# Kernel optimization log

Hardware: AMD Instinct MI355X
Metric: run time of the kernel (lower is better)

## Reference

```python
import jax, jax.numpy as jnp
import numpy as np
import math

B, H, N, D = 2, 16, 2048, 128
SM_SCALE = 1.0 / math.sqrt(D)


def setup_inputs() -> dict:
    key = jax.random.key(0)
    kq, kk, kv = jax.random.split(key, 3)
    q = jax.random.normal(kq, (B, H, N, D), dtype=jnp.float32)
    k = jax.random.normal(kk, (B, H, N, D), dtype=jnp.float32)
    v = jax.random.normal(kv, (B, H, N, D), dtype=jnp.float32)
    return {"q": q, "k": k, "v": v}


def reference(q, k, v):
    # RBF-kernel causal attention (non-softmax):
    #   logits_ij = -sm_scale * ||q_i - k_j||^2
    #            = 2*sm_scale*q_i.k_j - sm_scale*||q_i||^2 - sm_scale*||k_j||^2
    #   p = exp(logits) with causal mask (p_ij = 0 for j > i); out = p @ v
    sm_scale = jnp.float32(SM_SCALE)
    q_sq = sm_scale * jnp.sum(q * q, axis=-1)  # [B,H,N]
    k_sq = sm_scale * jnp.sum(k * k, axis=-1)  # [B,H,N]
    qk = jnp.einsum("bhmd,bhnd->bhmn", q, k)
    logits = (2.0 * sm_scale) * qk - q_sq[..., :, None] - k_sq[..., None, :]
    n = q.shape[2]
    causal = jnp.tril(jnp.ones((n, n), dtype=bool))
    logits = jnp.where(causal, logits, -jnp.inf)
    p = jnp.exp(logits)  # NOT normalized (non-softmax attention)
    out = jnp.einsum("bhmn,bhnd->bhmd", p, v)
    return out
```

## Files before the change

### kernel.cpp

```cpp
#include <hip/hip_runtime.h>
#include <math.h>


#define NSEQ 2048
#define DH   128
#define BHC  32
#define SM_SCALE 0.08838834764831845f

typedef __attribute__((ext_vector_type(8))) short    short8;
typedef __attribute__((ext_vector_type(8))) _Float16 half8;
typedef __attribute__((ext_vector_type(4))) short    short4_;
typedef __attribute__((ext_vector_type(4))) float    float4_;
typedef __attribute__((ext_vector_type(4))) unsigned uint4_;
typedef __attribute__((ext_vector_type(2))) unsigned uint2_;

#define KST 136
#define VST 72
#define PST 72

__device__ __forceinline__ short f2bf(float x){
  union{float f; unsigned u;} a; a.f=x;
  unsigned r = a.u + 0x7fffu + ((a.u>>16)&1u);
  return (short)(r>>16);
}
__device__ __forceinline__ float bf2f(short h){
  union{float f; unsigned u;} a; a.u=((unsigned)(unsigned short)h)<<16; return a.f;
}
__device__ __forceinline__ unsigned packbf(float a, float b){
  return (unsigned)(unsigned short)f2bf(a) | ((unsigned)(unsigned short)f2bf(b)<<16);
}

__global__ __launch_bounds__(256)
void prep_kv5(const float* __restrict__ kg, const float* __restrict__ vg,
              _Float16* __restrict__ khg, short* __restrict__ vtg,
              float* __restrict__ ksqg){
  __shared__ unsigned Vls[128*33];
  const int b = blockIdx.x, t = threadIdx.x;
  const int l = t & 63, wv = t >> 6;
  if(b < 1024){
    const int bh = b>>5, jt = b&31;
    const float4_* vb4 = (const float4_*)(vg + ((size_t)bh*NSEQ + (size_t)jt*64)*DH);
    #pragma unroll
    for(int i=0;i<8;++i){
      float4_ own = vb4[i*256 + t];
      float4_ par;
      par.x = __shfl_xor(own.x, 32); par.y = __shfl_xor(own.y, 32);
      par.z = __shfl_xor(own.z, 32); par.w = __shfl_xor(own.w, 32);
      const int hi = (l>>5)&1;
      unsigned w0 = hi ? packbf(par.z, own.z) : packbf(own.x, par.x);
      unsigned w1 = hi ? packbf(par.w, own.w) : packbf(own.y, par.y);
      const int dd = 4*(t&31) + 2*hi;
      const int j2 = 4*i + wv;
      Vls[dd*33 + j2]     = w0;
      Vls[(dd+1)*33 + j2] = w1;
    }
    __syncthreads();
    short* outp = vtg + ((size_t)(bh*32 + jt)*DH)*64;
    #pragma unroll
    for(int it=0; it<4; ++it){
      int idx = t + 256*it;
      int d = idx>>3, slot = idx&7;
      uint4_ o;
      o.x = Vls[d*33 + 4*slot];   o.y = Vls[d*33 + 4*slot+1];
      o.z = Vls[d*33 + 4*slot+2]; o.w = Vls[d*33 + 4*slot+3];
      *(uint4_*)(outp + d*64 + 8*slot) = o;
    }
  } else {
    const int kb = b - 1024;
    const float4_* kb4 = (const float4_*)(kg + (size_t)kb*64*DH);
    #pragma unroll
    for(int i=0;i<8;++i){
      float4_ x = kb4[i*256 + t];
      const int row = 64*kb + 8*i + (t>>5);
      const int d   = 4*(t&31);
      union{ _Float16 h[4]; uint2_ u; } pk;
      pk.h[0]=(_Float16)x.x; pk.h[1]=(_Float16)x.y;
      pk.h[2]=(_Float16)x.z; pk.h[3]=(_Float16)x.w;
      *(uint2_*)(khg + (size_t)row*DH + d) = pk.u;
      float ss = x.x*x.x + x.y*x.y + x.z*x.z + x.w*x.w;
      ss += __shfl_xor(ss,1);  ss += __shfl_xor(ss,2);
      ss += __shfl_xor(ss,4);  ss += __shfl_xor(ss,8);
      ss += __shfl_xor(ss,16);
      if((l&31)==0) ksqg[row] = SM_SCALE*ss;
    }
  }
}

__global__ __launch_bounds__(256,2)
void rbf_attn5(const float* __restrict__ qg,
               const _Float16* __restrict__ khg,
               const short* __restrict__ vtg,
               const float* __restrict__ ksqg,
               float* __restrict__ og){
  __shared__ short Kst[64*KST];
  __shared__ short Vst[128*VST];
  __shared__ short Pls[4*32*PST];
  __shared__ float ksLs[64];

  const int tid=threadIdx.x;
  const int w=tid>>6, l=tid&63;
  const int quad=l>>4, lr=l&15;
  const int bh=blockIdx.x, y=blockIdx.y;
  const int s = (y<8) ? y : 23-y;
  const int m_w   = (w<2) ? s : 31-s;
  const int qbase = 64*m_w + 32*(w&1);
  const int mb = 31-s;

  const float*    Qg = qg   + (size_t)bh*NSEQ*DH;
  const _Float16* Kh = khg  + (size_t)bh*NSEQ*DH;
  const short*    Vt = vtg  + (size_t)bh*32*DH*64;
  const float*    Ks = ksqg + (size_t)bh*NSEQ;
  float*          Og = og   + (size_t)bh*NSEQ*DH;
  short* Pw = Pls + w*32*PST;

  half8 qf[2][4];
  float qsq[2];
  #pragma unroll
  for(int rt=0;rt<2;++rt){
    const int qrow = qbase + 16*rt + lr;
    const float* qp = Qg + (size_t)qrow*DH + 8*quad;
    float ss=0.f;
    #pragma unroll
    for(int ks=0;ks<4;++ks){
      float4_ a = *(const float4_*)(qp + 32*ks);
      float4_ b = *(const float4_*)(qp + 32*ks + 4);
      half8 h;
      #pragma unroll
      for(int j=0;j<4;++j){
        h[j]   = (_Float16)a[j];
        h[j+4] = (_Float16)b[j];
        ss += a[j]*a[j] + b[j]*b[j];
      }
      qf[rt][ks]=h;
    }
    ss += __shfl_xor(ss,16);
    ss += __shfl_xor(ss,32);
    qsq[rt] = SM_SCALE*ss;
  }

  float4_ oacc[2][8];
  #pragma unroll
  for(int a=0;a<2;++a)
    #pragma unroll
    for(int b=0;b<8;++b) oacc[a][b] = (float4_)0.f;

  uint4_ kreg[4], vreg[4];
  float  kqreg = 0.f;
  {
    #pragma unroll
    for(int it=0;it<4;++it){
      int idx = tid + 256*it;
      int row = idx>>4, c = idx&15;
      kreg[it] = *(const uint4_*)(Kh + (size_t)row*DH + 8*c);
      int d = idx>>3, slot = idx&7;
      vreg[it] = *(const uint4_*)(Vt + (size_t)d*64 + 8*slot);
    }
    if(tid<64) kqreg = Ks[tid];
  }

  for(int jt=0; jt<=mb; ++jt){
    #pragma unroll
    for(int it=0;it<4;++it){
      int idx = tid + 256*it;
      int row = idx>>4, c = idx&15;
      *(uint4_*)&Kst[row*KST + 8*c] = kreg[it];
      int d = idx>>3, slot = idx&7;
      *(uint4_*)&Vst[d*VST + 8*slot] = vreg[it];
    }
    if(tid<64) ksLs[tid] = kqreg;
    __syncthreads();

    if(jt < mb){
      const int jc2 = (jt+1)*64;
      #pragma unroll
      for(int it=0;it<4;++it){
        int idx = tid + 256*it;
        int row = idx>>4, c = idx&15;
        kreg[it] = *(const uint4_*)(Kh + (size_t)(jc2+row)*DH + 8*c);
        int d = idx>>3, slot = idx&7;
        vreg[it] = *(const uint4_*)(Vt + ((size_t)(jt+1)*DH + d)*64 + 8*slot);
      }
      if(tid<64) kqreg = Ks[jc2 + tid];
    }

    if(jt <= m_w){
      float4_ sacc[2][4];
      #pragma unroll
      for(int a=0;a<2;++a)
        #pragma unroll
        for(int b=0;b<4;++b) sacc[a][b] = (float4_)0.f;

      #pragma unroll
      for(int ks=0;ks<4;++ks){
        half8 kf[4];
        #pragma unroll
        for(int ct=0;ct<4;++ct)
          kf[ct] = *(const half8*)&Kst[(16*ct+lr)*KST + 32*ks + 8*quad];
        #pragma unroll
        for(int rt=0;rt<2;++rt)
          #pragma unroll
          for(int ct=0;ct<4;++ct)
            sacc[rt][ct]=__builtin_amdgcn_mfma_f32_16x16x32_f16(kf[ct],qf[rt][ks],sacc[rt][ct],0,0,0);
      }

      const int jg0 = 64*jt;
      #pragma unroll
      for(int rt=0;rt<2;++rt){
        const int qrow = qbase + 16*rt + lr;
        const float qs = qsq[rt];
        #pragma unroll
        for(int ct=0;ct<4;++ct){
          float4_ kq = *(const float4_*)&ksLs[16*ct + 4*quad];
          const int j0 = jg0 + 16*ct + 4*quad;
          short4_ pw;
          #pragma unroll
          for(int r=0;r<4;++r){
            float logit = (2.f*SM_SCALE)*sacc[rt][ct][r] - qs - kq[r];
            float p = (j0 + r <= qrow) ? __expf(logit) : 0.f;
            pw[r] = f2bf(p);
          }
          *(short4_*)&Pw[(16*rt+lr)*PST + 16*ct + 4*quad] = pw;
        }
      }

      #pragma unroll
      for(int ks2=0;ks2<2;++ks2){
        short8 pf[2];
        #pragma unroll
        for(int rt=0;rt<2;++rt)
          pf[rt] = *(const short8*)&Pw[(16*rt+lr)*PST + 32*ks2 + 8*quad];
        #pragma unroll
        for(int ctv=0;ctv<8;++ctv){
          const short8 vf = *(const short8*)&Vst[(16*ctv+lr)*VST + 32*ks2 + 8*quad];
          #pragma unroll
          for(int rt=0;rt<2;++rt)
            oacc[rt][ctv]=__builtin_amdgcn_mfma_f32_16x16x32_bf16(pf[rt],vf,oacc[rt][ctv],0,0,0);
        }
      }
    }
    __syncthreads();
  }

  #pragma unroll
  for(int rt=0;rt<2;++rt)
    #pragma unroll
    for(int ctv=0;ctv<8;++ctv)
      #pragma unroll
      for(int r=0;r<4;++r){
        const int qrow = qbase + 16*rt + 4*quad + r;
        Og[(size_t)qrow*DH + 16*ctv + lr] = oacc[rt][ctv][r];
      }
}

#define KSTf 136
#define VSTf 36
#define PSTf 72

__global__ __launch_bounds__(256,2)
void rbf_attn_mfma(const float* __restrict__ qg, const float* __restrict__ kg,
                   const float* __restrict__ vg, float* __restrict__ og){
  __shared__ short    Khi[64*KSTf];
  __shared__ short    Klo[64*KSTf];
  __shared__ unsigned VP [128*VSTf];
  __shared__ short    Pfb[64*PSTf];
  __shared__ float    qsq_s[64];
  __shared__ float    ksq_s[64];

  const int tid=threadIdx.x;
  const int w=tid>>6, l=tid&63;
  const int wr=w>>1, wc=w&1;
  const int quad=l>>4, lr=l&15;
  const int bh=blockIdx.x, yp=blockIdx.y;

  const float* Qg = qg + (size_t)bh*NSEQ*DH;
  const float* Kg = kg + (size_t)bh*NSEQ*DH;
  const float* Vg = vg + (size_t)bh*NSEQ*DH;
  float*       Og = og + (size_t)bh*NSEQ*DH;

  for(int pass=0;pass<2;++pass){
    const int m = pass ? (31-yp) : yp;
    __syncthreads();
    short8 qhf[2][4], qlf[2][4];
    #pragma unroll
    for(int rt=0;rt<2;++rt){
      const int grow = m*64 + 32*wr + 16*rt + lr;
      const float* qp = Qg + (size_t)grow*DH + 8*quad;
      float ss=0.f;
      #pragma unroll
      for(int ks=0;ks<4;++ks){
        float4_ a = *(const float4_*)(qp + 32*ks);
        float4_ b = *(const float4_*)(qp + 32*ks + 4);
        short8 hi, lo;
        #pragma unroll
        for(int j=0;j<4;++j){
          float fa=a[j], fb=b[j];
          short ha=f2bf(fa); hi[j]=ha;   lo[j]=f2bf(fa-bf2f(ha));
          short hb=f2bf(fb); hi[j+4]=hb; lo[j+4]=f2bf(fb-bf2f(hb));
          ss += fa*fa + fb*fb;
        }
        qhf[rt][ks]=hi; qlf[rt][ks]=lo;
      }
      ss += __shfl_xor(ss,16);
      ss += __shfl_xor(ss,32);
      if(wc==0 && quad==0) qsq_s[32*wr+16*rt+lr] = SM_SCALE*ss;
    }
    float4_ oacc[2][4];
    #pragma unroll
    for(int a=0;a<2;++a)
      #pragma unroll
      for(int b=0;b<4;++b) oacc[a][b] = (float4_)0.f;

    const int ntiles = m+1;
    for(int jt=0;jt<ntiles;++jt){
      const int jc = jt*64;
      __syncthreads();
      #pragma unroll
      for(int it=0;it<4;++it){
        const int i = tid + 256*it;
        const int row = i>>4, c0 = 8*(i&15);
        const float* kp = Kg + (size_t)(jc+row)*DH + c0;
        float4_ a = *(const float4_*)kp;
        float4_ b = *(const float4_*)(kp+4);
        short8 hi, lo;
        float ss=0.f;
        #pragma unroll
        for(int j=0;j<4;++j){
          float fa=a[j], fb=b[j];
          short ha=f2bf(fa); hi[j]=ha;   lo[j]=f2bf(fa-bf2f(ha));
          short hb=f2bf(fb); hi[j+4]=hb; lo[j+4]=f2bf(fb-bf2f(hb));
          ss += fa*fa + fb*fb;
        }
        ss += __shfl_xor(ss,1); ss += __shfl_xor(ss,2);
        ss += __shfl_xor(ss,4); ss += __shfl_xor(ss,8);
        if(lr==0) ksq_s[row] = SM_SCALE*ss;
        *(short8*)&Khi[row*KSTf + c0] = hi;
        *(short8*)&Klo[row*KSTf + c0] = lo;
      }
      #pragma unroll
      for(int it=0;it<4;++it){
        const int u = tid + 256*it;
        const int d = u & 127, jg = u >> 7;
        const float* vp = Vg + (size_t)(jc + 8*jg)*DH + d;
        float vv[8];
        #pragma unroll
        for(int jj=0;jj<8;++jj) vv[jj] = vp[(size_t)jj*DH];
        uint4_ pk;
        #pragma unroll
        for(int p2=0;p2<4;++p2)
          pk[p2] = (unsigned)(unsigned short)f2bf(vv[2*p2]) |
                   ((unsigned)(unsigned short)f2bf(vv[2*p2+1])<<16);
        *(uint4_*)&VP[d*VSTf + 4*jg] = pk;
      }
      __syncthreads();
      float4_ sacc[2][2];
      #pragma unroll
      for(int a=0;a<2;++a)
        #pragma unroll
        for(int b=0;b<2;++b) sacc[a][b] = (float4_)0.f;
      #pragma unroll
      for(int ks=0;ks<4;++ks){
        short8 khf[2], klf[2];
        #pragma unroll
        for(int ct=0;ct<2;++ct){
          const int off = (32*wc + 16*ct + lr)*KSTf + 32*ks + 8*quad;
          khf[ct] = *(const short8*)&Khi[off];
          klf[ct] = *(const short8*)&Klo[off];
        }
        #pragma unroll
        for(int rt=0;rt<2;++rt)
          #pragma unroll
          for(int ct=0;ct<2;++ct){
            sacc[rt][ct]=__builtin_amdgcn_mfma_f32_16x16x32_bf16(qhf[rt][ks],khf[ct],sacc[rt][ct],0,0,0);
            sacc[rt][ct]=__builtin_amdgcn_mfma_f32_16x16x32_bf16(qhf[rt][ks],klf[ct],sacc[rt][ct],0,0,0);
            sacc[rt][ct]=__builtin_amdgcn_mfma_f32_16x16x32_bf16(qlf[rt][ks],khf[ct],sacc[rt][ct],0,0,0);
          }
      }
      #pragma unroll
      for(int rt=0;rt<2;++rt){
        float qs[4];
        #pragma unroll
        for(int r=0;r<4;++r) qs[r]=qsq_s[32*wr+16*rt+4*quad+r];
        #pragma unroll
        for(int ct=0;ct<2;++ct){
          const float ksq = ksq_s[32*wc+16*ct+lr];
          const int colg = jc + 32*wc+16*ct+lr;
          #pragma unroll
          for(int r=0;r<4;++r){
            const int rowg = m*64 + 32*wr+16*rt+4*quad+r;
            float logit = (2.f*SM_SCALE)*sacc[rt][ct][r] - qs[r] - ksq;
            float p = (colg<=rowg)? __expf(logit) : 0.f;
            Pfb[(32*wr+16*rt+4*quad+r)*PSTf + 32*wc+16*ct+lr] = f2bf(p);
          }
        }
      }
      __syncthreads();
      #pragma unroll
      for(int ks2=0;ks2<2;++ks2){
        short8 pf[2];
        #pragma unroll
        for(int rt=0;rt<2;++rt)
          pf[rt] = *(const short8*)&Pfb[(32*wr+16*rt+lr)*PSTf + 32*ks2 + 8*quad];
        #pragma unroll
        for(int ctv=0;ctv<4;++ctv){
          const int d = 64*wc + 16*ctv + lr;
          const short8 vfb = *(const short8*)((const short*)VP + d*(2*VSTf) + 32*ks2 + 8*quad);
          #pragma unroll
          for(int rt=0;rt<2;++rt)
            oacc[rt][ctv]=__builtin_amdgcn_mfma_f32_16x16x32_bf16(pf[rt],vfb,oacc[rt][ctv],0,0,0);
        }
      }
    }
    #pragma unroll
    for(int rt=0;rt<2;++rt)
      #pragma unroll
      for(int ctv=0;ctv<4;++ctv)
        #pragma unroll
        for(int r=0;r<4;++r){
          const int rowg = m*64 + 32*wr + 16*rt + 4*quad + r;
          Og[(size_t)rowg*DH + 64*wc + 16*ctv + lr] = oacc[rt][ctv][r];
        }
  }
}

extern "C" void kernel_launch(void* const* d_in, const int* in_sizes, int n_in,
                              void* d_out, int out_size, void* d_ws, size_t ws_size,
                              hipStream_t stream) {
  const float* q = (const float*)d_in[0];
  const float* k = (const float*)d_in[1];
  const float* v = (const float*)d_in[2];
  float* out = (float*)d_out;

  const size_t nElem = (size_t)BHC*NSEQ*DH;
  const size_t need  = nElem*2*sizeof(short) + (size_t)BHC*NSEQ*sizeof(float);

  if(ws_size >= need){
    _Float16* khg = (_Float16*)d_ws;
    short*    vtg = (short*)(khg + nElem);
    float*    ksqg = (float*)(vtg + nElem);
    prep_kv5<<<2048, 256, 0, stream>>>(k, v, khg, vtg, ksqg);
    rbf_attn5<<<dim3(BHC,16), 256, 0, stream>>>(q, khg, vtg, ksqg, out);
  } else {
    rbf_attn_mfma<<<dim3(BHC,16), 256, 0, stream>>>(q, k, v, out);
  }
}
```

Before: 213.2 us.

## Split attention into one 64-row query block per workgroup with 16 rows per wave

The attention grid goes from 16 to 32 blocks per head. Each workgroup now handles one 64-row query tile, ordered heaviest first, and each wave owns 16 query rows, replacing the paired light/heavy tile scheme where waves held 32 rows. Halving per-wave accumulators lowers register pressure, allowing 3 workgroups per CU. The change also uses the hardware v_cvt_pk_bf16_f32 conversion in place of software rounding, and raises wave priority (s_setprio) around the MFMA sections. In exchange, each K/V tile loaded into LDS is reused by fewer query rows, so K/V traffic and barriers per unit of work increase.

```diff
diff --git a/kernel.cpp b/kernel.cpp
--- a/kernel.cpp
+++ b/kernel.cpp
@@ -28,6 +28,11 @@
 }
 __device__ __forceinline__ unsigned packbf(float a, float b){
   return (unsigned)(unsigned short)f2bf(a) | ((unsigned)(unsigned short)f2bf(b)<<16);
+}
+__device__ __forceinline__ unsigned cvtpk_bf16(float a, float b){
+  unsigned r;
+  asm("v_cvt_pk_bf16_f32 %0, %1, %2" : "=v"(r) : "v"(a), "v"(b));
+  return r;
 }
 
 __global__ __launch_bounds__(256)
@@ -86,38 +91,35 @@
   }
 }
 
-__global__ __launch_bounds__(256,2)
-void rbf_attn5(const float* __restrict__ qg,
+__global__ __launch_bounds__(256,3)
+void rbf_attn6(const float* __restrict__ qg,
                const _Float16* __restrict__ khg,
                const short* __restrict__ vtg,
                const float* __restrict__ ksqg,
                float* __restrict__ og){
   __shared__ short Kst[64*KST];
   __shared__ short Vst[128*VST];
-  __shared__ short Pls[4*32*PST];
+  __shared__ short Pls[4*16*PST];
   __shared__ float ksLs[64];
 
   const int tid=threadIdx.x;
   const int w=tid>>6, l=tid&63;
   const int quad=l>>4, lr=l&15;
-  const int bh=blockIdx.x, y=blockIdx.y;
-  const int s = (y<8) ? y : 23-y;
-  const int m_w   = (w<2) ? s : 31-s;
-  const int qbase = 64*m_w + 32*(w&1);
-  const int mb = 31-s;
+  const int bh=blockIdx.x;
+  const int mq = 31 - blockIdx.y;
+  const int qbase = 64*mq + 16*w;
 
   const float*    Qg = qg   + (size_t)bh*NSEQ*DH;
   const _Float16* Kh = khg  + (size_t)bh*NSEQ*DH;
   const short*    Vt = vtg  + (size_t)bh*32*DH*64;
   const float*    Ks = ksqg + (size_t)bh*NSEQ;
   float*          Og = og   + (size_t)bh*NSEQ*DH;
-  short* Pw = Pls + w*32*PST;
-
-  half8 qf[2][4];
-  float qsq[2];
-  #pragma unroll
-  for(int rt=0;rt<2;++rt){
-    const int qrow = qbase + 16*rt + lr;
+  short* Pw = Pls + w*16*PST;
+
+  half8 qf[4];
+  float qsq;
+  {
+    const int qrow = qbase + lr;
     const float* qp = Qg + (size_t)qrow*DH + 8*quad;
     float ss=0.f;
     #pragma unroll
@@ -131,18 +133,16 @@
         h[j+4] = (_Float16)b[j];
         ss += a[j]*a[j] + b[j]*b[j];
       }
-      qf[rt][ks]=h;
+      qf[ks]=h;
     }
     ss += __shfl_xor(ss,16);
     ss += __shfl_xor(ss,32);
-    qsq[rt] = SM_SCALE*ss;
-  }
-
-  float4_ oacc[2][8];
+    qsq = SM_SCALE*ss;
+  }
+
+  float4_ oacc[8];
   #pragma unroll
-  for(int a=0;a<2;++a)
-    #pragma unroll
-    for(int b=0;b<8;++b) oacc[a][b] = (float4_)0.f;
+  for(int b2=0;b2<8;++b2) oacc[b2] = (float4_)0.f;
 
   uint4_ kreg[4], vreg[4];
   float  kqreg = 0.f;
@@ -158,7 +158,7 @@
     if(tid<64) kqreg = Ks[tid];
   }
 
-  for(int jt=0; jt<=mb; ++jt){
+  for(int jt=0; jt<=mq; ++jt){
     #pragma unroll
     for(int it=0;it<4;++it){
       int idx = tid + 256*it;
@@ -170,7 +170,7 @@
     if(tid<64) ksLs[tid] = kqreg;
     __syncthreads();
 
-    if(jt < mb){
+    if(jt < mq){
       const int jc2 = (jt+1)*64;
       #pragma unroll
       for(int it=0;it<4;++it){
@@ -183,73 +183,65 @@
       if(tid<64) kqreg = Ks[jc2 + tid];
     }
 
-    if(jt <= m_w){
-      float4_ sacc[2][4];
-      #pragma unroll
-      for(int a=0;a<2;++a)
-        #pragma unroll
-        for(int b=0;b<4;++b) sacc[a][b] = (float4_)0.f;
-
-      #pragma unroll
-      for(int ks=0;ks<4;++ks){
-        half8 kf[4];
-        #pragma unroll
-        for(int ct=0;ct<4;++ct)
-          kf[ct] = *(const half8*)&Kst[(16*ct+lr)*KST + 32*ks + 8*quad];
-        #pragma unroll
-        for(int rt=0;rt<2;++rt)
-          #pragma unroll
-          for(int ct=0;ct<4;++ct)
-            sacc[rt][ct]=__builtin_amdgcn_mfma_f32_16x16x32_f16(kf[ct],qf[rt][ks],sacc[rt][ct],0,0,0);
-      }
-
+    float4_ sacc[4];
+    #pragma unroll
+    for(int ct=0;ct<4;++ct) sacc[ct] = (float4_)0.f;
+
+    __builtin_amdgcn_s_setprio(1);
+    #pragma unroll
+    for(int ks=0;ks<4;++ks){
+      half8 kf[4];
+      #pragma unroll
+      for(int ct=0;ct<4;++ct)
+        kf[ct] = *(const half8*)&Kst[(16*ct+lr)*KST + 32*ks + 8*quad];
+      #pragma unroll
+      for(int ct=0;ct<4;++ct)
+        sacc[ct]=__builtin_amdgcn_mfma_f32_16x16x32_f16(kf[ct],qf[ks],sacc[ct],0,0,0);
+    }
+    __builtin_amdgcn_s_setprio(0);
+
+    {
       const int jg0 = 64*jt;
-      #pragma unroll
-      for(int rt=0;rt<2;++rt){
-        const int qrow = qbase + 16*rt + lr;
-        const float qs = qsq[rt];
-        #pragma unroll
-        for(int ct=0;ct<4;++ct){
-          float4_ kq = *(const float4_*)&ksLs[16*ct + 4*quad];
-          const int j0 = jg0 + 16*ct + 4*quad;
-          short4_ pw;
-          #pragma unroll
-          for(int r=0;r<4;++r){
-            float logit = (2.f*SM_SCALE)*sacc[rt][ct][r] - qs - kq[r];
-            float p = (j0 + r <= qrow) ? __expf(logit) : 0.f;
-            pw[r] = f2bf(p);
-          }
-          *(short4_*)&Pw[(16*rt+lr)*PST + 16*ct + 4*quad] = pw;
-        }
-      }
-
-      #pragma unroll
-      for(int ks2=0;ks2<2;++ks2){
-        short8 pf[2];
-        #pragma unroll
-        for(int rt=0;rt<2;++rt)
-          pf[rt] = *(const short8*)&Pw[(16*rt+lr)*PST + 32*ks2 + 8*quad];
-        #pragma unroll
-        for(int ctv=0;ctv<8;++ctv){
-          const short8 vf = *(const short8*)&Vst[(16*ctv+lr)*VST + 32*ks2 + 8*quad];
-          #pragma unroll
-          for(int rt=0;rt<2;++rt)
-            oacc[rt][ctv]=__builtin_amdgcn_mfma_f32_16x16x32_bf16(pf[rt],vf,oacc[rt][ctv],0,0,0);
-        }
-      }
-    }
+      const int qrow = qbase + lr;
+      #pragma unroll
+      for(int ct=0;ct<4;++ct){
+        float4_ kq = *(const float4_*)&ksLs[16*ct + 4*quad];
+        const int j0 = jg0 + 16*ct + 4*quad;
+        float p[4];
+        #pragma unroll
+        for(int r=0;r<4;++r){
+          float logit = (2.f*SM_SCALE)*sacc[ct][r] - qsq - kq[r];
+          p[r] = (j0 + r <= qrow) ? __expf(logit) : 0.f;
+        }
+        uint2_ pw;
+        pw.x = cvtpk_bf16(p[0], p[1]);
+        pw.y = cvtpk_bf16(p[2], p[3]);
+        *(uint2_*)&Pw[lr*PST + 16*ct + 4*quad] = pw;
+      }
+    }
+
+    __builtin_amdgcn_s_setprio(1);
+    #pragma unroll
+    for(int ks2=0;ks2<2;++ks2){
+      const short8 pf = *(const short8*)&Pw[lr*PST + 32*ks2 + 8*quad];
+      #pragma unroll
+      for(int ctv=0;ctv<8;++ctv){
+        const short8 vf = *(const short8*)&Vst[(16*ctv+lr)*VST + 32*ks2 + 8*quad];
+        oacc[ctv]=__builtin_amdgcn_mfma_f32_16x16x32_bf16(pf,vf,oacc[ctv],0,0,0);
+      }
+    }
+    __builtin_amdgcn_s_setprio(0);
+
     __syncthreads();
   }
 
   #pragma unroll
-  for(int rt=0;rt<2;++rt)
-    #pragma unroll
-    for(int ctv=0;ctv<8;++ctv)
-      #pragma unroll
-      for(int r=0;r<4;++r){
-        const int qrow = qbase + 16*rt + 4*quad + r;
-        Og[(size_t)qrow*DH + 16*ctv + lr] = oacc[rt][ctv][r];
-      }
+  for(int ctv=0;ctv<8;++ctv)
+    #pragma unroll
+    for(int r=0;r<4;++r){
+      const int qrow = qbase + 4*quad + r;
+      Og[(size_t)qrow*DH + 16*ctv + lr] = oacc[ctv][r];
+    }
 }
 
 #define KSTf 136
@@ -438,7 +430,7 @@
     short*    vtg = (short*)(khg + nElem);
     float*    ksqg = (float*)(vtg + nElem);
     prep_kv5<<<2048, 256, 0, stream>>>(k, v, khg, vtg, ksqg);
-    rbf_attn5<<<dim3(BHC,16), 256, 0, stream>>>(q, khg, vtg, ksqg, out);
+    rbf_attn6<<<dim3(BHC,32), 256, 0, stream>>>(q, khg, vtg, ksqg, out);
   } else {
     rbf_attn_mfma<<<dim3(BHC,16), 256, 0, stream>>>(q, k, v, out);
   }
```

Measured after the change: 196.8 us. 1.08x faster.
